# Kernel optimization log

Measured on AMD Instinct MI355X. Metric: run time of the kernel, lower is better.

Reference implementation:

```python
import jax, jax.numpy as jnp
import numpy as np

NUM_HEADS = 8
LN_EPS = 1e-5


def _positional_encoding(pos_index, d_pe):
    # standard sinusoidal PE, positions start at 1; sin on even cols, cos on odd cols
    pos = pos_index.astype(jnp.float32)[:, None]                      # [N,1]
    freqs = jnp.exp(jnp.arange(0, d_pe, 2, dtype=jnp.float32) * (-np.log(10000.0) / d_pe))
    ang = pos * freqs                                                 # [N, d_pe//2]
    return jnp.stack([jnp.sin(ang), jnp.cos(ang)], axis=-1).reshape(pos.shape[0], d_pe)


def setup_inputs() -> dict:
    EMB, POS, DEV, B = 512, 64, 448, 64
    lengths = np.where(np.arange(B) % 2 == 0, 128, 256)               # ragged group sizes
    state_index = jnp.asarray(np.concatenate([[0], np.cumsum(lengths)]), dtype=jnp.int32)
    total = int(lengths.sum())                                        # 12288
    ks = jax.random.split(jax.random.key(0), 5)
    in_dim = DEV + POS
    return {
        "states": jax.random.normal(ks[0], (total, DEV), jnp.float32),
        "state_index": state_index,
        "W1": jax.random.normal(ks[1], (EMB, in_dim), jnp.float32) / np.sqrt(in_dim),
        "b1": jnp.zeros((EMB,), jnp.float32),
        "in_w": jax.random.normal(ks[2], (3 * EMB, EMB), jnp.float32) / np.sqrt(EMB),
        "in_b": jnp.zeros((3 * EMB,), jnp.float32),
        "out_w": jax.random.normal(ks[3], (EMB, EMB), jnp.float32) / np.sqrt(EMB),
        "out_b": jnp.zeros((EMB,), jnp.float32),
        "gamma": jnp.ones((EMB,), jnp.float32),
        "beta": jnp.zeros((EMB,), jnp.float32),
    }


def reference(states, state_index, W1, b1, in_w, in_b, out_w, out_b, gamma, beta):
    # --- static ragged bookkeeping from the int offsets (host-side) ---
    si = np.asarray(state_index)
    lengths = si[1:] - si[:-1]
    b = len(lengths)
    max_d = int(lengths.max())
    batch_index = jnp.asarray(np.repeat(np.arange(b), lengths), jnp.int32)   # [N]
    pos_np = np.concatenate([np.arange(1, l + 1) for l in lengths])
    pos_index = jnp.asarray(pos_np, jnp.int32)                               # [N], 1-based
    seq_idx = pos_index - 1                                                  # [N], 0-based slot

    E = W1.shape[0]
    d_pe = W1.shape[1] - states.shape[1]
    hd = E // NUM_HEADS

    # embedding MLP
    pe = _positional_encoding(pos_index, d_pe)
    x = jnp.concatenate([states, pe], axis=1)                                # [N, dev+pe]
    emb = jax.nn.leaky_relu(x @ W1.T + b1, 0.01)                             # [N, E]

    # scatter ragged tokens into padded [b, max_d, E] (zero filler, as in _reshape)
    dense = jnp.zeros((b, max_d, E), emb.dtype).at[batch_index, seq_idx].set(emb)

    # MultiheadAttention (batch_first, no padding mask -- faithful to original)
    qkv = dense @ in_w.T + in_b                                              # [b, md, 3E]
    q, k, v = jnp.split(qkv, 3, axis=-1)
    q = q.reshape(b, max_d, NUM_HEADS, hd)
    k = k.reshape(b, max_d, NUM_HEADS, hd)
    v = v.reshape(b, max_d, NUM_HEADS, hd)
    scores = jnp.einsum("bqhd,bkhd->bhqk", q, k) / np.sqrt(hd)
    attn = jax.nn.softmax(scores, axis=-1)
    ctx = jnp.einsum("bhqk,bkhd->bqhd", attn, v).reshape(b, max_d, E)
    mha_out = ctx @ out_w.T + out_b

    # residual + LayerNorm
    res = mha_out + dense
    mu = res.mean(axis=-1, keepdims=True)
    var = ((res - mu) ** 2).mean(axis=-1, keepdims=True)
    norm = (res - mu) / jnp.sqrt(var + LN_EPS) * gamma + beta

    # gather valid rows back out and concat with pre-attention embeddings
    sel = norm[batch_index, seq_idx]                                         # [N, E]
    return jnp.concatenate([emb, sel], axis=1)                               # [N, 2E]
```

## Files before the change

kernel.cpp:

```cpp
#include <hip/hip_runtime.h>

typedef unsigned short u16;
typedef __attribute__((ext_vector_type(8))) short bf16x8;
typedef __attribute__((ext_vector_type(4))) float f32x4;

__device__ __forceinline__ float bf2f(u16 u) {
    union { unsigned int i; float f; } v; v.i = ((unsigned int)u) << 16; return v.f;
}
__device__ __forceinline__ u16 f2bf(float f) {
    union { float f; unsigned int i; } v; v.f = f;
    unsigned int x = v.i;
    return (u16)((x + 0x7FFFu + ((x >> 16) & 1u)) >> 16);
}

__device__ __forceinline__ bool probe_f32(const void* gamma) {
    return *(const unsigned int*)gamma == 0x3F800000u;
}
__device__ __forceinline__ float load1(const void* p, int i, bool f32) {
    return f32 ? ((const float*)p)[i] : bf2f(((const u16*)p)[i]);
}
__device__ __forceinline__ uint4 load8(const void* p, size_t e, bool f32) {
    if (f32) {
        const float* q = (const float*)p + e;
        float4 a = *(const float4*)q;
        float4 b = *(const float4*)(q + 4);
        uint4 r; u16* rp = (u16*)&r;
        rp[0] = f2bf(a.x); rp[1] = f2bf(a.y); rp[2] = f2bf(a.z); rp[3] = f2bf(a.w);
        rp[4] = f2bf(b.x); rp[5] = f2bf(b.y); rp[6] = f2bf(b.z); rp[7] = f2bf(b.w);
        return r;
    }
    return *(const uint4*)((const u16*)p + e);
}
__device__ __forceinline__ void store1(void* p, size_t i, float v, bool f32) {
    if (f32) ((float*)p)[i] = v;
    else     ((u16*)p)[i] = f2bf(v);
}

__device__ __forceinline__ void glds16(const u16* g, u16* l) {
    __builtin_amdgcn_global_load_lds(
        (const __attribute__((address_space(1))) void*)g,
        (__attribute__((address_space(3))) void*)l, 16, 0, 0);
}

#define NTOK   12288
#define BATCH  64
#define MAXD   256
#define EMB    512
#define DEV    448

__global__ __launch_bounds__(64) void prep_all(
        const void* __restrict__ W1, const void* __restrict__ in_w,
        const void* __restrict__ out_w, const void* __restrict__ b1,
        const void* __restrict__ in_b, const void* __restrict__ out_b,
        const void* __restrict__ gamma, const void* __restrict__ beta,
        u16* __restrict__ W1b, u16* __restrict__ in_wb, u16* __restrict__ out_wb,
        float* __restrict__ b1f, float* __restrict__ in_bf, float* __restrict__ out_bf,
        float* __restrict__ gf, float* __restrict__ bfv)
{
    bool f32 = probe_f32(gamma);
    int r = blockIdx.x, t = threadIdx.x;
    if (r < 512) {
        *(uint4*)&W1b[(size_t)r * 512 + t * 8] = load8(W1, (size_t)r * 512 + t * 8, f32);
    } else if (r < 2048) {
        int rc = r - 512;
        int h = rc / 192, rr = rc - h * 192;
        int part = rr >> 6, d = rc & 63;
        int orig = part * 512 + h * 64 + d;
        *(uint4*)&in_wb[(size_t)rc * 512 + t * 8] = load8(in_w, (size_t)orig * 512 + t * 8, f32);
    } else if (r < 2560) {
        int rc = r - 2048;
        *(uint4*)&out_wb[(size_t)rc * 512 + t * 8] = load8(out_w, (size_t)rc * 512 + t * 8, f32);
    } else if (r == 2560) {
        #pragma unroll
        for (int u = 0; u < 8; ++u) b1f[t * 8 + u] = load1(b1, t * 8 + u, f32);
    } else if (r < 2564) {
        int base = (r - 2561) * 512 + t * 8;
        #pragma unroll
        for (int u = 0; u < 8; ++u) {
            int j = base + u;
            int h = j / 192, rr = j - h * 192;
            int part = rr >> 6, d = j & 63;
            int orig = part * 512 + h * 64 + d;
            in_bf[j] = load1(in_b, orig, f32);
        }
    } else if (r == 2564) {
        #pragma unroll
        for (int u = 0; u < 8; ++u) out_bf[t * 8 + u] = load1(out_b, t * 8 + u, f32);
    } else if (r == 2565) {
        #pragma unroll
        for (int u = 0; u < 8; ++u) gf[t * 8 + u] = load1(gamma, t * 8 + u, f32);
    } else {
        #pragma unroll
        for (int u = 0; u < 8; ++u) bfv[t * 8 + u] = load1(beta, t * 8 + u, f32);
    }
}

__global__ __launch_bounds__(64) void xin_build(
        const void* __restrict__ states, const int* __restrict__ si,
        u16* __restrict__ xin, const void* __restrict__ gamma)
{
    __shared__ int ssi[65];
    bool f32 = probe_f32(gamma);
    int n = blockIdx.x, t = threadIdx.x;
    ssi[t] = si[t];
    if (t == 0) ssi[64] = si[64];
    __syncthreads();
    int lo = 0, hi = 64;
    while (hi - lo > 1) { int mid = (lo + hi) >> 1; if (ssi[mid] <= n) lo = mid; else hi = mid; }
    float pos = (float)(n - ssi[lo] + 1);
    if (t < 56) {
        *(uint4*)&xin[(size_t)n * 512 + t * 8] = load8(states, (size_t)n * DEV + t * 8, f32);
    } else {
        int j0 = (t - 56) * 8;
        uint4 vu; u16* vp = (u16*)&vu;
        #pragma unroll
        for (int jj = 0; jj < 8; ++jj) {
            int j = j0 + jj;
            int i = j >> 1;
            float freq = __expf(-0.2878231366f * (float)i);
            float ang = pos * freq;
            vp[jj] = f2bf((j & 1) ? cosf(ang) : sinf(ang));
        }
        *(uint4*)&xin[(size_t)n * 512 + DEV + j0] = vu;
    }
}

template<int MODE>
__global__ __launch_bounds__(256) void gemm_glds(
        const u16* __restrict__ A, const u16* __restrict__ B,
        const float* __restrict__ bias, u16* __restrict__ C)
{
    constexpr int LDC = (MODE == 1) ? 1536 : 512;
    __shared__ __align__(16) u16 Ash[128 * 32];
    __shared__ __align__(16) u16 Bsh[128 * 32];

    int tid = threadIdx.x;
    int bm0 = blockIdx.y * 128, bn0 = blockIdx.x * 128;
    int lane = tid & 63, w = tid >> 6;
    int wm = (w >> 1) * 64, wn = (w & 1) * 64;
    int q = lane >> 4, m16 = lane & 15;
    int lr = lane >> 2, lc = (lane & 3) * 8;

    f32x4 acc[4][4];
    #pragma unroll
    for (int i = 0; i < 4; ++i)
        #pragma unroll
        for (int j = 0; j < 4; ++j) acc[i][j] = (f32x4){0.f, 0.f, 0.f, 0.f};

    const u16* Ab = A + (size_t)(bm0 + w * 16 + lr) * 512 + lc;
    const u16* Bb = B + (size_t)(bn0 + w * 16 + lr) * 512 + lc;
    u16* AshW = &Ash[(w * 16) * 32];
    u16* BshW = &Bsh[(w * 16) * 32];

    for (int k0 = 0; k0 < 512; k0 += 32) {
        __syncthreads();
        glds16(Ab + k0, AshW);
        glds16(Ab + (size_t)64 * 512 + k0, AshW + 64 * 32);
        glds16(Bb + k0, BshW);
        glds16(Bb + (size_t)64 * 512 + k0, BshW + 64 * 32);
        __syncthreads();
        bf16x8 af[4], bfr[4];
        #pragma unroll
        for (int i = 0; i < 4; ++i)
            af[i] = *(const bf16x8*)&Ash[(wm + i * 16 + m16) * 32 + q * 8];
        #pragma unroll
        for (int j = 0; j < 4; ++j)
            bfr[j] = *(const bf16x8*)&Bsh[(wn + j * 16 + m16) * 32 + q * 8];
        #pragma unroll
        for (int i = 0; i < 4; ++i)
            #pragma unroll
            for (int j = 0; j < 4; ++j)
                acc[i][j] = __builtin_amdgcn_mfma_f32_16x16x32_bf16(af[i], bfr[j], acc[i][j], 0, 0, 0);
    }

    #pragma unroll
    for (int i = 0; i < 4; ++i) {
        #pragma unroll
        for (int j = 0; j < 4; ++j) {
            int c = bn0 + wn + j * 16 + m16;
            float bv = bias[c];
            #pragma unroll
            for (int r = 0; r < 4; ++r) {
                int row = bm0 + wm + i * 16 + q * 4 + r;
                float v = acc[i][j][r] + bv;
                if constexpr (MODE == 0) v = v >= 0.f ? v : 0.01f * v;
                C[(size_t)row * LDC + c] = f2bf(v);
            }
        }
    }
}

template<int LEN>
__global__ __launch_bounds__(512) void attn_mfma(
        const u16* __restrict__ qkv, const int* __restrict__ si,
        const float* __restrict__ in_bf, u16* __restrict__ ctx)
{
    constexpr int NT   = LEN / 16;
    constexpr int KS   = LEN / 32;
    constexpr int NPAD = 256 - LEN;
    constexpr int KSTR = 72;
    constexpr int VTS  = LEN + 8;

    __shared__ __align__(16) u16 Ksh[LEN * KSTR];
    __shared__ __align__(16) u16 Vt[64 * VTS];
    __shared__ __align__(16) u16 PshBuf[8 * 16 * VTS];
    __shared__ float kbsh[64];
    __shared__ float apsh[8][16];

    int h = blockIdx.x;
    int b = blockIdx.y * 2 + (LEN == 256 ? 1 : 0);
    int tid = threadIdx.x;
    int tok0 = si[b];
    int bb = h * 192;

    if (NPAD > 0 && tid < 64) kbsh[tid] = in_bf[bb + 64 + tid];

    constexpr int nIter = LEN * 8 / 512;
    #pragma unroll
    for (int it = 0; it < nIter; ++it) {
        int idx = tid + it * 512;
        int row = idx >> 3, c8 = (idx & 7) * 8;
        const u16* src = qkv + (size_t)(tok0 + row) * 1536 + bb;
        uint4 kv = *(const uint4*)(src + 64 + c8);
        *(uint4*)&Ksh[row * KSTR + c8] = kv;
        uint4 vv = *(const uint4*)(src + 128 + c8);
        const unsigned int* vw = (const unsigned int*)&vv;
        #pragma unroll
        for (int u = 0; u < 4; ++u)
            *(unsigned int*)&PshBuf[row * 66 + c8 + 2 * u] = vw[u];
    }
    __syncthreads();
    constexpr int SHIFT = (LEN == 256) ? 7 : 6;
    constexpr int tIter = (64 * (LEN / 2)) / 512;
    #pragma unroll
    for (int it = 0; it < tIter; ++it) {
        int idx = tid + it * 512;
        int d = idx >> SHIFT, kp = idx & (LEN / 2 - 1);
        unsigned int lo = PshBuf[(2 * kp) * 66 + d];
        unsigned int hi = PshBuf[(2 * kp + 1) * 66 + d];
        *(unsigned int*)&Vt[d * VTS + 2 * kp] = (hi << 16) | lo;
    }
    __syncthreads();

    int lane = tid & 63, w = tid >> 6;
    int m16 = lane & 15, quad = lane >> 4;
    int wq = w >> 2, wr = w & 3;
    int qt = (LEN == 256) ? blockIdx.z * 2 + wq : wq;
    u16* Psh = &PshBuf[w * 16 * VTS];

    int qrow = qt * 64 + wr * 16 + m16;
    const u16* qptr = qkv + (size_t)(tok0 + qrow) * 1536 + bb;
    bf16x8 aq0 = *(const bf16x8*)(qptr + quad * 8);
    bf16x8 aq1 = *(const bf16x8*)(qptr + 32 + quad * 8);

    if (NPAD > 0) {
        float apv = 0.f;
        #pragma unroll
        for (int j = 0; j < 8; ++j) {
            apv += bf2f((u16)aq0[j]) * kbsh[quad * 8 + j];
            apv += bf2f((u16)aq1[j]) * kbsh[32 + quad * 8 + j];
        }
        apv += __shfl_xor(apv, 16);
        apv += __shfl_xor(apv, 32);
        if (lane < 16) apsh[w][lane] = apv * 0.125f;
    }

    f32x4 sfr[NT];
    #pragma unroll
    for (int nt = 0; nt < NT; ++nt) sfr[nt] = (f32x4){0.f, 0.f, 0.f, 0.f};
    #pragma unroll
    for (int nt = 0; nt < NT; ++nt) {
        const u16* kr = &Ksh[(nt * 16 + m16) * KSTR + quad * 8];
        bf16x8 bk0 = *(const bf16x8*)(kr);
        bf16x8 bk1 = *(const bf16x8*)(kr + 32);
        sfr[nt] = __builtin_amdgcn_mfma_f32_16x16x32_bf16(aq0, bk0, sfr[nt], 0, 0, 0);
        sfr[nt] = __builtin_amdgcn_mfma_f32_16x16x32_bf16(aq1, bk1, sfr[nt], 0, 0, 0);
    }

    float pwv[4];
    #pragma unroll
    for (int reg = 0; reg < 4; ++reg) {
        float mx = -3.0e38f;
        #pragma unroll
        for (int nt = 0; nt < NT; ++nt) mx = fmaxf(mx, sfr[nt][reg]);
        mx *= 0.125f;
        float ap = 0.f;
        if (NPAD > 0) { ap = apsh[w][quad * 4 + reg]; mx = fmaxf(mx, ap); }
        #pragma unroll
        for (int off = 8; off >= 1; off >>= 1) mx = fmaxf(mx, __shfl_xor(mx, off));
        float p[NT];
        float sum = 0.f;
        #pragma unroll
        for (int nt = 0; nt < NT; ++nt) {
            p[nt] = __expf(sfr[nt][reg] * 0.125f - mx);
            sum += p[nt];
        }
        #pragma unroll
        for (int off = 8; off >= 1; off >>= 1) sum += __shfl_xor(sum, off);
        float padw = (NPAD > 0) ? (float)NPAD * __expf(ap - mx) : 0.f;
        float inv = __frcp_rn(sum + padw);
        pwv[reg] = padw * inv;
        #pragma unroll
        for (int nt = 0; nt < NT; ++nt)
            Psh[(quad * 4 + reg) * VTS + nt * 16 + m16] = f2bf(p[nt] * inv);
    }

    f32x4 ob[4];
    #pragma unroll
    for (int nt = 0; nt < 4; ++nt) ob[nt] = (f32x4){0.f, 0.f, 0.f, 0.f};
    #pragma unroll
    for (int ks = 0; ks < KS; ++ks) {
        bf16x8 af = *(const bf16x8*)&Psh[m16 * VTS + ks * 32 + quad * 8];
        #pragma unroll
        for (int nt = 0; nt < 4; ++nt) {
            bf16x8 bv = *(const bf16x8*)&Vt[(nt * 16 + m16) * VTS + ks * 32 + quad * 8];
            ob[nt] = __builtin_amdgcn_mfma_f32_16x16x32_bf16(af, bv, ob[nt], 0, 0, 0);
        }
    }

    int orow = tok0 + qt * 64 + wr * 16;
    #pragma unroll
    for (int nt = 0; nt < 4; ++nt) {
        int d = nt * 16 + m16;
        float vbv = (NPAD > 0) ? in_bf[bb + 128 + d] : 0.f;
        #pragma unroll
        for (int reg = 0; reg < 4; ++reg) {
            float val = ob[nt][reg];
            if (NPAD > 0) val += pwv[reg] * vbv;
            ctx[(size_t)(orow + quad * 4 + reg) * 512 + h * 64 + d] = f2bf(val);
        }
    }
}

__global__ __launch_bounds__(64) void ln_out(
        const u16* __restrict__ mha, const u16* __restrict__ emb,
        const float* __restrict__ gf, const float* __restrict__ bfv,
        void* __restrict__ out, const void* __restrict__ gamma)
{
    int n = blockIdx.x, lane = threadIdx.x;
    bool f32 = probe_f32(gamma);
    float r[8], e[8];
    float sum = 0.f, sq = 0.f;
    #pragma unroll
    for (int u = 0; u < 8; ++u) {
        int c = u * 64 + lane;
        e[u] = bf2f(emb[(size_t)n * EMB + c]);
        r[u] = bf2f(mha[(size_t)n * EMB + c]) + e[u];
        sum += r[u];
        sq += r[u] * r[u];
    }
    #pragma unroll
    for (int off = 32; off >= 1; off >>= 1) {
        sum += __shfl_xor(sum, off);
        sq  += __shfl_xor(sq, off);
    }
    float mu = sum * (1.f / 512.f);
    float var = sq * (1.f / 512.f) - mu * mu;
    float rstd = rsqrtf(var + 1e-5f);
    #pragma unroll
    for (int u = 0; u < 8; ++u) {
        int c = u * 64 + lane;
        store1(out, (size_t)n * 1024 + c, e[u], f32);
        store1(out, (size_t)n * 1024 + 512 + c, (r[u] - mu) * rstd * gf[c] + bfv[c], f32);
    }
}

extern "C" void kernel_launch(void* const* d_in, const int* in_sizes, int n_in,
                              void* d_out, int out_size, void* d_ws, size_t ws_size,
                              hipStream_t stream) {
    const void* states = d_in[0];
    const int*  si     = (const int*)d_in[1];
    const void* W1     = d_in[2];
    const void* b1     = d_in[3];
    const void* in_w   = d_in[4];
    const void* in_b   = d_in[5];
    const void* out_w  = d_in[6];
    const void* out_b  = d_in[7];
    const void* gamma  = d_in[8];
    const void* beta   = d_in[9];

    char* ws = (char*)d_ws;
    u16* emb    = (u16*)(ws);
    u16* xin    = (u16*)(ws + 12582912);
    u16* mha    = xin;
    u16* qkvF   = (u16*)(ws + 25165824);
    u16* W1b    = (u16*)(ws + 62914560);
    u16* in_wb  = (u16*)(ws + 63438848);
    u16* out_wb = (u16*)(ws + 65011712);
    float* b1f    = (float*)(ws + 65536000);
    float* in_bf  = (float*)(ws + 65538048);
    float* out_bf = (float*)(ws + 65544192);
    float* gf     = (float*)(ws + 65546240);
    float* bfv    = (float*)(ws + 65548288);

    u16* ctx = (u16*)d_out;

    prep_all<<<2567, 64, 0, stream>>>(W1, in_w, out_w, b1, in_b, out_b, gamma, beta,
                                      W1b, in_wb, out_wb, b1f, in_bf, out_bf, gf, bfv);
    xin_build<<<NTOK, 64, 0, stream>>>(states, si, xin, gamma);
    gemm_glds<0><<<dim3(4, 96), 256, 0, stream>>>(xin, W1b, b1f, emb);
    gemm_glds<1><<<dim3(12, 96), 256, 0, stream>>>(emb, in_wb, in_bf, qkvF);
    attn_mfma<128><<<dim3(8, 32, 1), 512, 0, stream>>>(qkvF, si, in_bf, ctx);
    attn_mfma<256><<<dim3(8, 32, 2), 512, 0, stream>>>(qkvF, si, in_bf, ctx);
    gemm_glds<2><<<dim3(4, 96), 256, 0, stream>>>(ctx, out_wb, out_bf, mha);
    ln_out<<<NTOK, 64, 0, stream>>>(mha, emb, gf, bfv, d_out, gamma);
}
```

Before: 203.8 us.

## Merge prep and xin kernels, stage GEMM epilogue via LDS, vectorize LayerNorm I/O

Folds the weight-conversion kernel and the input-build kernel into one launch, removing one kernel launch and its boundary. The GEMM epilogue now packs results to bf16 with a hardware convert instruction and stages them through a per-wave LDS tile, so each row is written to global memory as coalesced 16-byte stores instead of scattered 2-byte stores. The LayerNorm output kernel switches to contiguous 8-element vector loads and stores. The GEMM uses more shared memory, which may reduce occupancy, and the packed convert may round differently from the manual rounding it replaces.

```diff
diff --git a/kernel.cpp b/kernel.cpp
--- a/kernel.cpp
+++ b/kernel.cpp
@@ -11,6 +11,11 @@
     union { float f; unsigned int i; } v; v.f = f;
     unsigned int x = v.i;
     return (u16)((x + 0x7FFFu + ((x >> 16) & 1u)) >> 16);
+}
+__device__ __forceinline__ unsigned int f2bf_pk(float a, float b) {
+    unsigned int r;
+    asm("v_cvt_pk_bf16_f32 %0, %1, %2" : "=v"(r) : "v"(a), "v"(b));
+    return r;
 }
 
 __device__ __forceinline__ bool probe_f32(const void* gamma) {
@@ -31,10 +36,6 @@
     }
     return *(const uint4*)((const u16*)p + e);
 }
-__device__ __forceinline__ void store1(void* p, size_t i, float v, bool f32) {
-    if (f32) ((float*)p)[i] = v;
-    else     ((u16*)p)[i] = f2bf(v);
-}
 
 __device__ __forceinline__ void glds16(const u16* g, u16* l) {
     __builtin_amdgcn_global_load_lds(
@@ -48,80 +49,78 @@
 #define EMB    512
 #define DEV    448
 
-__global__ __launch_bounds__(64) void prep_all(
+__global__ __launch_bounds__(64) void prep_xin(
+        const void* __restrict__ states, const int* __restrict__ si,
         const void* __restrict__ W1, const void* __restrict__ in_w,
         const void* __restrict__ out_w, const void* __restrict__ b1,
         const void* __restrict__ in_b, const void* __restrict__ out_b,
         const void* __restrict__ gamma, const void* __restrict__ beta,
         u16* __restrict__ W1b, u16* __restrict__ in_wb, u16* __restrict__ out_wb,
         float* __restrict__ b1f, float* __restrict__ in_bf, float* __restrict__ out_bf,
-        float* __restrict__ gf, float* __restrict__ bfv)
+        float* __restrict__ gf, float* __restrict__ bfv, u16* __restrict__ xin)
 {
     bool f32 = probe_f32(gamma);
-    int r = blockIdx.x, t = threadIdx.x;
-    if (r < 512) {
-        *(uint4*)&W1b[(size_t)r * 512 + t * 8] = load8(W1, (size_t)r * 512 + t * 8, f32);
-    } else if (r < 2048) {
-        int rc = r - 512;
-        int h = rc / 192, rr = rc - h * 192;
-        int part = rr >> 6, d = rc & 63;
-        int orig = part * 512 + h * 64 + d;
-        *(uint4*)&in_wb[(size_t)rc * 512 + t * 8] = load8(in_w, (size_t)orig * 512 + t * 8, f32);
-    } else if (r < 2560) {
-        int rc = r - 2048;
-        *(uint4*)&out_wb[(size_t)rc * 512 + t * 8] = load8(out_w, (size_t)rc * 512 + t * 8, f32);
-    } else if (r == 2560) {
-        #pragma unroll
-        for (int u = 0; u < 8; ++u) b1f[t * 8 + u] = load1(b1, t * 8 + u, f32);
-    } else if (r < 2564) {
-        int base = (r - 2561) * 512 + t * 8;
-        #pragma unroll
-        for (int u = 0; u < 8; ++u) {
-            int j = base + u;
-            int h = j / 192, rr = j - h * 192;
-            int part = rr >> 6, d = j & 63;
+    int t = threadIdx.x;
+    if (blockIdx.x < 2567) {
+        int r = blockIdx.x;
+        if (r < 512) {
+            *(uint4*)&W1b[(size_t)r * 512 + t * 8] = load8(W1, (size_t)r * 512 + t * 8, f32);
+        } else if (r < 2048) {
+            int rc = r - 512;
+            int h = rc / 192, rr = rc - h * 192;
+            int part = rr >> 6, d = rc & 63;
             int orig = part * 512 + h * 64 + d;
-            in_bf[j] = load1(in_b, orig, f32);
-        }
-    } else if (r == 2564) {
-        #pragma unroll
-        for (int u = 0; u < 8; ++u) out_bf[t * 8 + u] = load1(out_b, t * 8 + u, f32);
-    } else if (r == 2565) {
-        #pragma unroll
-        for (int u = 0; u < 8; ++u) gf[t * 8 + u] = load1(gamma, t * 8 + u, f32);
+            *(uint4*)&in_wb[(size_t)rc * 512 + t * 8] = load8(in_w, (size_t)orig * 512 + t * 8, f32);
+        } else if (r < 2560) {
+            int rc = r - 2048;
+            *(uint4*)&out_wb[(size_t)rc * 512 + t * 8] = load8(out_w, (size_t)rc * 512 + t * 8, f32);
+        } else if (r == 2560) {
+            #pragma unroll
+            for (int u = 0; u < 8; ++u) b1f[t * 8 + u] = load1(b1, t * 8 + u, f32);
+        } else if (r < 2564) {
+            int base = (r - 2561) * 512 + t * 8;
+            #pragma unroll
+            for (int u = 0; u < 8; ++u) {
+                int j = base + u;
+                int h = j / 192, rr = j - h * 192;
+                int part = rr >> 6, d = j & 63;
+                int orig = part * 512 + h * 64 + d;
+                in_bf[j] = load1(in_b, orig, f32);
+            }
+        } else if (r == 2564) {
+            #pragma unroll
+            for (int u = 0; u < 8; ++u) out_bf[t * 8 + u] = load1(out_b, t * 8 + u, f32);
+        } else if (r == 2565) {
+            #pragma unroll
+            for (int u = 0; u < 8; ++u) gf[t * 8 + u] = load1(gamma, t * 8 + u, f32);
+        } else {
+            #pragma unroll
+            for (int u = 0; u < 8; ++u) bfv[t * 8 + u] = load1(beta, t * 8 + u, f32);
+        }
     } else {
-        #pragma unroll
-        for (int u = 0; u < 8; ++u) bfv[t * 8 + u] = load1(beta, t * 8 + u, f32);
-    }
-}
-
-__global__ __launch_bounds__(64) void xin_build(
-        const void* __restrict__ states, const int* __restrict__ si,
-        u16* __restrict__ xin, const void* __restrict__ gamma)
-{
-    __shared__ int ssi[65];
-    bool f32 = probe_f32(gamma);
-    int n = blockIdx.x, t = threadIdx.x;
-    ssi[t] = si[t];
-    if (t == 0) ssi[64] = si[64];
-    __syncthreads();
-    int lo = 0, hi = 64;
-    while (hi - lo > 1) { int mid = (lo + hi) >> 1; if (ssi[mid] <= n) lo = mid; else hi = mid; }
-    float pos = (float)(n - ssi[lo] + 1);
-    if (t < 56) {
-        *(uint4*)&xin[(size_t)n * 512 + t * 8] = load8(states, (size_t)n * DEV + t * 8, f32);
-    } else {
-        int j0 = (t - 56) * 8;
-        uint4 vu; u16* vp = (u16*)&vu;
-        #pragma unroll
-        for (int jj = 0; jj < 8; ++jj) {
-            int j = j0 + jj;
-            int i = j >> 1;
-            float freq = __expf(-0.2878231366f * (float)i);
-            float ang = pos * freq;
-            vp[jj] = f2bf((j & 1) ? cosf(ang) : sinf(ang));
-        }
-        *(uint4*)&xin[(size_t)n * 512 + DEV + j0] = vu;
+        int n = blockIdx.x - 2567;
+        __shared__ int ssi[65];
+        ssi[t] = si[t];
+        if (t == 0) ssi[64] = si[64];
+        __syncthreads();
+        int lo = 0, hi = 64;
+        while (hi - lo > 1) { int mid = (lo + hi) >> 1; if (ssi[mid] <= n) lo = mid; else hi = mid; }
+        float pos = (float)(n - ssi[lo] + 1);
+        if (t < 56) {
+            *(uint4*)&xin[(size_t)n * 512 + t * 8] = load8(states, (size_t)n * DEV + t * 8, f32);
+        } else {
+            int j0 = (t - 56) * 8;
+            uint4 vu; u16* vp = (u16*)&vu;
+            #pragma unroll
+            for (int jj = 0; jj < 8; ++jj) {
+                int j = j0 + jj;
+                int i = j >> 1;
+                float freq = __expf(-0.2878231366f * (float)i);
+                float ang = pos * freq;
+                vp[jj] = f2bf((j & 1) ? cosf(ang) : sinf(ang));
+            }
+            *(uint4*)&xin[(size_t)n * 512 + DEV + j0] = vu;
+        }
     }
 }
 
@@ -133,6 +132,7 @@
     constexpr int LDC = (MODE == 1) ? 1536 : 512;
     __shared__ __align__(16) u16 Ash[128 * 32];
     __shared__ __align__(16) u16 Bsh[128 * 32];
+    __shared__ __align__(16) u16 Csh[4 * 32 * 72];
 
     int tid = threadIdx.x;
     int bm0 = blockIdx.y * 128, bn0 = blockIdx.x * 128;
@@ -173,19 +173,47 @@
                 acc[i][j] = __builtin_amdgcn_mfma_f32_16x16x32_bf16(af[i], bfr[j], acc[i][j], 0, 0, 0);
     }
 
-    #pragma unroll
-    for (int i = 0; i < 4; ++i) {
-        #pragma unroll
-        for (int j = 0; j < 4; ++j) {
-            int c = bn0 + wn + j * 16 + m16;
-            float bv = bias[c];
-            #pragma unroll
-            for (int r = 0; r < 4; ++r) {
-                int row = bm0 + wm + i * 16 + q * 4 + r;
-                float v = acc[i][j][r] + bv;
-                if constexpr (MODE == 0) v = v >= 0.f ? v : 0.01f * v;
-                C[(size_t)row * LDC + c] = f2bf(v);
+    u16* cw = &Csh[w * 32 * 72];
+    float bv[4];
+    #pragma unroll
+    for (int j = 0; j < 4; ++j) bv[j] = bias[bn0 + wn + j * 16 + m16];
+
+    int rrl = lane >> 3;
+    int rcc = (lane & 7) * 8;
+
+    #pragma unroll
+    for (int ch = 0; ch < 2; ++ch) {
+        #pragma unroll
+        for (int ii = 0; ii < 2; ++ii) {
+            int i = ch * 2 + ii;
+            #pragma unroll
+            for (int j = 0; j < 4; ++j) {
+                float v0 = acc[i][j][0] + bv[j];
+                float v1 = acc[i][j][1] + bv[j];
+                float v2 = acc[i][j][2] + bv[j];
+                float v3 = acc[i][j][3] + bv[j];
+                if constexpr (MODE == 0) {
+                    v0 = v0 >= 0.f ? v0 : 0.01f * v0;
+                    v1 = v1 >= 0.f ? v1 : 0.01f * v1;
+                    v2 = v2 >= 0.f ? v2 : 0.01f * v2;
+                    v3 = v3 >= 0.f ? v3 : 0.01f * v3;
+                }
+                unsigned int pk01 = f2bf_pk(v0, v1);
+                unsigned int pk23 = f2bf_pk(v2, v3);
+                int rb = ii * 16 + q * 4;
+                int cl = j * 16 + m16;
+                cw[(rb + 0) * 72 + cl] = (u16)pk01;
+                cw[(rb + 1) * 72 + cl] = (u16)(pk01 >> 16);
+                cw[(rb + 2) * 72 + cl] = (u16)pk23;
+                cw[(rb + 3) * 72 + cl] = (u16)(pk23 >> 16);
             }
+        }
+        #pragma unroll
+        for (int p = 0; p < 4; ++p) {
+            int row_l = p * 8 + rrl;
+            uint4 v = *(const uint4*)&cw[row_l * 72 + rcc];
+            int grow = bm0 + wm + ch * 32 + row_l;
+            *(uint4*)&C[(size_t)grow * LDC + bn0 + wn + rcc] = v;
         }
     }
 }
@@ -339,13 +367,17 @@
 {
     int n = blockIdx.x, lane = threadIdx.x;
     bool f32 = probe_f32(gamma);
-    float r[8], e[8];
+    size_t base = (size_t)n * EMB + lane * 8;
+    uint4 ev = *(const uint4*)&emb[base];
+    uint4 mv = *(const uint4*)&mha[base];
+    const u16* ep = (const u16*)&ev;
+    const u16* mp = (const u16*)&mv;
+    float e[8], r[8];
     float sum = 0.f, sq = 0.f;
     #pragma unroll
     for (int u = 0; u < 8; ++u) {
-        int c = u * 64 + lane;
-        e[u] = bf2f(emb[(size_t)n * EMB + c]);
-        r[u] = bf2f(mha[(size_t)n * EMB + c]) + e[u];
+        e[u] = bf2f(ep[u]);
+        r[u] = bf2f(mp[u]) + e[u];
         sum += r[u];
         sq += r[u] * r[u];
     }
@@ -357,11 +389,35 @@
     float mu = sum * (1.f / 512.f);
     float var = sq * (1.f / 512.f) - mu * mu;
     float rstd = rsqrtf(var + 1e-5f);
-    #pragma unroll
-    for (int u = 0; u < 8; ++u) {
-        int c = u * 64 + lane;
-        store1(out, (size_t)n * 1024 + c, e[u], f32);
-        store1(out, (size_t)n * 1024 + 512 + c, (r[u] - mu) * rstd * gf[c] + bfv[c], f32);
+
+    float4 g0 = *(const float4*)(gf + lane * 8);
+    float4 g1 = *(const float4*)(gf + lane * 8 + 4);
+    float4 be0 = *(const float4*)(bfv + lane * 8);
+    float4 be1 = *(const float4*)(bfv + lane * 8 + 4);
+    float g[8] = {g0.x, g0.y, g0.z, g0.w, g1.x, g1.y, g1.z, g1.w};
+    float bb[8] = {be0.x, be0.y, be0.z, be0.w, be1.x, be1.y, be1.z, be1.w};
+    float o[8];
+    #pragma unroll
+    for (int u = 0; u < 8; ++u) o[u] = (r[u] - mu) * rstd * g[u] + bb[u];
+
+    if (f32) {
+        float* op = (float*)out + (size_t)n * 1024 + lane * 8;
+        *(float4*)(op)           = make_float4(e[0], e[1], e[2], e[3]);
+        *(float4*)(op + 4)       = make_float4(e[4], e[5], e[6], e[7]);
+        *(float4*)(op + 512)     = make_float4(o[0], o[1], o[2], o[3]);
+        *(float4*)(op + 516)     = make_float4(o[4], o[5], o[6], o[7]);
+    } else {
+        u16* op = (u16*)out + (size_t)n * 1024 + lane * 8;
+        uint4 v1, v2;
+        unsigned int* w1 = (unsigned int*)&v1;
+        unsigned int* w2 = (unsigned int*)&v2;
+        #pragma unroll
+        for (int u = 0; u < 4; ++u) {
+            w1[u] = f2bf_pk(e[2 * u], e[2 * u + 1]);
+            w2[u] = f2bf_pk(o[2 * u], o[2 * u + 1]);
+        }
+        *(uint4*)(op)       = v1;
+        *(uint4*)(op + 512) = v2;
     }
 }
 
@@ -395,9 +451,9 @@
 
     u16* ctx = (u16*)d_out;
 
-    prep_all<<<2567, 64, 0, stream>>>(W1, in_w, out_w, b1, in_b, out_b, gamma, beta,
-                                      W1b, in_wb, out_wb, b1f, in_bf, out_bf, gf, bfv);
-    xin_build<<<NTOK, 64, 0, stream>>>(states, si, xin, gamma);
+    prep_xin<<<2567 + NTOK, 64, 0, stream>>>(states, si, W1, in_w, out_w, b1, in_b, out_b,
+                                             gamma, beta, W1b, in_wb, out_wb,
+                                             b1f, in_bf, out_bf, gf, bfv, xin);
     gemm_glds<0><<<dim3(4, 96), 256, 0, stream>>>(xin, W1b, b1f, emb);
     gemm_glds<1><<<dim3(12, 96), 256, 0, stream>>>(emb, in_wb, in_bf, qkvF);
     attn_mfma<128><<<dim3(8, 32, 1), 512, 0, stream>>>(qkvF, si, in_bf, ctx);
```

Result: no change. 201.0 us (-1.4%).
